# Performance work log

Measured on AMD Instinct MI355X. Metric: run time of the kernel, lower is better.

Reference implementation:

```python
import jax, jax.numpy as jnp
import numpy as np

L = 32            # num_layers
R = 16            # lora_rank
P = L * 7         # 224 projections
D = 256           # encoder d_model
H = 4             # encoder heads
HD = D // H
FF = 2048         # TransformerEncoderLayer default dim_feedforward
PED = 512         # proj_embed_dim
HID = 4096
KV = 8 * (4096 // 32)   # 1024
INTER = 11008
VOCAB = 50000
NEG = -1e9

# projection index groups within the P=7*L ordering [q,k,v,o,gate,up,down]
IDX_A_HID = jnp.asarray((np.arange(L)[:, None] * 7 + np.array([0, 1, 2, 3, 4, 5])).reshape(-1))  # in_dim=4096
IDX_A_INT = jnp.asarray(np.arange(L) * 7 + 6)                                                    # in_dim=11008
IDX_B_HID = jnp.asarray((np.arange(L)[:, None] * 7 + np.array([0, 3, 6])).reshape(-1))           # out_dim=4096
IDX_B_KV  = jnp.asarray((np.arange(L)[:, None] * 7 + np.array([1, 2])).reshape(-1))              # out_dim=1024
IDX_B_INT = jnp.asarray((np.arange(L)[:, None] * 7 + np.array([4, 5])).reshape(-1))              # out_dim=11008


def _ln(x, g, b, eps=1e-5):
    m = jnp.mean(x, -1, keepdims=True)
    v = jnp.mean((x - m) ** 2, -1, keepdims=True)
    return (x - m) * jax.lax.rsqrt(v + eps) * g + b


def _enc_layer(x, pad, qw, qb, ow, ob, g1, b1, f1w, f1b, f2w, f2b, g2, b2):
    # post-norm TransformerEncoderLayer (torch default), relu FFN, eval mode (no dropout)
    Bsz, S, _ = x.shape
    qkv = x @ qw.T + qb                                  # [B,S,3D]
    q, k, v = jnp.split(qkv, 3, axis=-1)
    hd = lambda t: t.reshape(Bsz, S, H, HD).transpose(0, 2, 1, 3)
    q, k, v = hd(q), hd(k), hd(v)
    s = jnp.einsum('bhqd,bhkd->bhqk', q, k) / jnp.asarray(np.sqrt(HD), x.dtype)
    s = jnp.where(pad[:, None, None, :], NEG, s)
    a = jax.nn.softmax(s, -1)
    o = jnp.einsum('bhqk,bhkd->bhqd', a, v).transpose(0, 2, 1, 3).reshape(Bsz, S, D)
    x = _ln(x + o @ ow.T + ob, g1, b1)
    f = jax.nn.relu(x @ f1w.T + f1b) @ f2w.T + f2b
    return _ln(x + f, g2, b2)


def _forward(condition_ids, attention_mask, embed_table, enc_qkv_w, enc_qkv_b, enc_out_w, enc_out_b,
             enc_ln1_g, enc_ln1_b, enc_ff1_w, enc_ff1_b, enc_ff2_w, enc_ff2_b, enc_ln2_g, enc_ln2_b,
             proj_w, proj_b, a1_w, a1_b, a2_w, a2_b, b1_w, b1_b, b2_w, b2_b, scales):
    Bsz = condition_ids.shape[0]
    x = embed_table[condition_ids]                       # [B,S,256]
    pad = attention_mask == 0                            # key padding mask (~attention_mask)
    for l in range(3):
        x = _enc_layer(x, pad, enc_qkv_w[l], enc_qkv_b[l], enc_out_w[l], enc_out_b[l],
                       enc_ln1_g[l], enc_ln1_b[l], enc_ff1_w[l], enc_ff1_b[l],
                       enc_ff2_w[l], enc_ff2_b[l], enc_ln2_g[l], enc_ln2_b[l])
    am = attention_mask.astype(x.dtype)
    pooled = (x * am[..., None]).sum(1) / jnp.clip(am.sum(1, keepdims=True), 1.0)   # masked mean pool
    pe = (pooled @ proj_w.T + proj_b).reshape(Bsz, P, PED)                          # [B,224,512]

    def dec(w1, b1_, w2, b2_):
        return jax.nn.gelu(pe @ w1.T + b1_, approximate=False) @ w2.T + b2_

    A_base = dec(a1_w, a1_b, a2_w, a2_b).reshape(Bsz, P, R, 64)   # [B,P,r,64]
    B_base = dec(b1_w, b1_b, b2_w, b2_b).reshape(Bsz, P, 64, R)   # [B,P,64,r]
    sa, sb = scales[:, 0], scales[:, 1]

    def tile_A(idx, in_d):
        # all in_dims divisible by 64 => repeat(in_d//64+1)[:, :in_d] == exact tiling
        a = A_base[:, idx] * sa[idx][None, :, None, None]
        return jnp.tile(a, (1, 1, 1, in_d // 64))

    def tile_B(idx, out_d):
        b = B_base[:, idx] * sb[idx][None, :, None, None]
        return jnp.tile(b, (1, 1, out_d // 64, 1))

    return (tile_A(IDX_A_HID, HID), tile_A(IDX_A_INT, INTER),
            tile_B(IDX_B_HID, HID), tile_B(IDX_B_KV, KV), tile_B(IDX_B_INT, INTER))


def setup_inputs() -> dict:
    key = jax.random.key(0)
    ks = iter(jax.random.split(key, 40))
    rn = lambda shape, s=0.02: jax.random.normal(next(ks), shape, jnp.float32) * s
    Bsz, S = 4, 128
    return {
        'condition_ids': jax.random.randint(next(ks), (Bsz, S), 0, VOCAB),
        'attention_mask': jnp.ones((Bsz, S), jnp.int32),
        'embed_table': rn((VOCAB, D)),
        'enc_qkv_w': rn((3, 3 * D, D)), 'enc_qkv_b': rn((3, 3 * D)),
        'enc_out_w': rn((3, D, D)), 'enc_out_b': rn((3, D)),
        'enc_ln1_g': jnp.ones((3, D)), 'enc_ln1_b': jnp.zeros((3, D)),
        'enc_ff1_w': rn((3, FF, D)), 'enc_ff1_b': rn((3, FF)),
        'enc_ff2_w': rn((3, D, FF)), 'enc_ff2_b': rn((3, D)),
        'enc_ln2_g': jnp.ones((3, D)), 'enc_ln2_b': jnp.zeros((3, D)),
        'proj_w': rn((P * PED, D)), 'proj_b': rn((P * PED,)),
        'a1_w': rn((D, PED)), 'a1_b': rn((D,)),
        'a2_w': rn((R * 64, D)), 'a2_b': rn((R * 64,)),
        'b1_w': rn((D, PED)), 'b1_b': rn((D,)),
        'b2_w': rn((R * 64, D)), 'b2_b': rn((R * 64,)),
        'scales': jnp.full((P, 2), 0.01, jnp.float32),
    }


def reference(condition_ids, attention_mask, embed_table, enc_qkv_w, enc_qkv_b, enc_out_w, enc_out_b,
              enc_ln1_g, enc_ln1_b, enc_ff1_w, enc_ff1_b, enc_ff2_w, enc_ff2_b, enc_ln2_g, enc_ln2_b,
              proj_w, proj_b, a1_w, a1_b, a2_w, a2_b, b1_w, b1_b, b2_w, b2_b, scales):
    return _forward(condition_ids, attention_mask, embed_table, enc_qkv_w, enc_qkv_b, enc_out_w, enc_out_b,
                    enc_ln1_g, enc_ln1_b, enc_ff1_w, enc_ff1_b, enc_ff2_w, enc_ff2_b, enc_ln2_g, enc_ln2_b,
                    proj_w, proj_b, a1_w, a1_b, a2_w, a2_b, b1_w, b1_b, b2_w, b2_b, scales)
```

## Files before the change

kernel.cpp:

```cpp
#include <hip/hip_runtime.h>
#include <hip/hip_bf16.h>

typedef unsigned short u16;
typedef unsigned int u32;
typedef __attribute__((ext_vector_type(8))) short short8;
typedef __attribute__((ext_vector_type(4))) float floatx4;

__device__ __forceinline__ u16 f2bf(float f) {
  u32 x = __float_as_uint(f);
  x += 0x7FFFu + ((x >> 16) & 1u);
  return (u16)(x >> 16);
}
__device__ __forceinline__ u32 pk2(float lo, float hi) {
  return (u32)f2bf(lo) | ((u32)f2bf(hi) << 16);
}

__global__ void embed_kernel(const int* __restrict__ ids, const float* __restrict__ emb,
                             float* __restrict__ x) {
  int tok = blockIdx.x, d = threadIdx.x;
  x[tok * 256 + d] = emb[(size_t)ids[tok] * 256 + d];
}

template <int ACT, int SPLIT>
__global__ __launch_bounds__(256) void mfma_gemm_kernel(const float* __restrict__ A,
    const float* __restrict__ W, const float* __restrict__ bias, float* __restrict__ C,
    int M, int N, int K, int KS, int pstride) {
  __shared__ u16 Abf[64 * 32];
  __shared__ u16 Wbf[64 * 32];
  const int t = threadIdx.x;
  const int m0 = blockIdx.x * 64, n0 = blockIdx.y * 64;
  const int kz = blockIdx.z;
  const int srow = t >> 2, skc = (t & 3) * 8;
  const int w = t >> 6, lane = t & 63;
  const int q = lane >> 4, rr = lane & 15;
  floatx4 acc[4];
#pragma unroll
  for (int i = 0; i < 4; ++i) acc[i] = (floatx4){0.f, 0.f, 0.f, 0.f};

  const int kbeg = kz * KS, kend = kbeg + KS;
  for (int k0 = kbeg; k0 < kend; k0 += 32) {
    const float* ga = A + (size_t)(m0 + srow) * K + k0 + skc;
    const float* gw = W + (size_t)(n0 + srow) * K + k0 + skc;
    float4 a0 = *(const float4*)ga;
    float4 a1 = *(const float4*)(ga + 4);
    float4 w0 = *(const float4*)gw;
    float4 w1 = *(const float4*)(gw + 4);
    uint4 pa, pw;
    pa.x = pk2(a0.x, a0.y); pa.y = pk2(a0.z, a0.w);
    pa.z = pk2(a1.x, a1.y); pa.w = pk2(a1.z, a1.w);
    pw.x = pk2(w0.x, w0.y); pw.y = pk2(w0.z, w0.w);
    pw.z = pk2(w1.x, w1.y); pw.w = pk2(w1.z, w1.w);
    __syncthreads();
    *(uint4*)&Abf[srow * 32 + skc] = pa;
    *(uint4*)&Wbf[srow * 32 + skc] = pw;
    __syncthreads();
    short8 af = *(short8*)&Abf[(w * 16 + rr) * 32 + q * 8];
#pragma unroll
    for (int ct = 0; ct < 4; ++ct) {
      short8 bf = *(short8*)&Wbf[(ct * 16 + rr) * 32 + q * 8];
      acc[ct] = __builtin_amdgcn_mfma_f32_16x16x32_bf16(af, bf, acc[ct], 0, 0, 0);
    }
  }

  float* dst = SPLIT ? (C + (size_t)kz * pstride) : C;
#pragma unroll
  for (int ct = 0; ct < 4; ++ct) {
    int col = n0 + ct * 16 + rr;
#pragma unroll
    for (int r = 0; r < 4; ++r) {
      int row = m0 + w * 16 + q * 4 + r;
      float v = acc[ct][r];
      if (!SPLIT) {
        v += bias[col];
        if (ACT == 1) v = fmaxf(v, 0.f);
        if (ACT == 2) v = 0.5f * v * (1.f + erff(v * 0.70710678118654752f));
      }
      dst[(size_t)row * N + col] = v;
    }
  }
}

template <int ACT>
__global__ void red_bias_act_kernel(const float* __restrict__ parts, int nparts, int pstride,
                                    const float* __restrict__ bias, float* __restrict__ dst, int N) {
  int idx = blockIdx.x * 256 + threadIdx.x;
  float v = bias[idx % N];
  for (int p = 0; p < nparts; ++p) v += parts[(size_t)p * pstride + idx];
  if (ACT == 1) v = fmaxf(v, 0.f);
  if (ACT == 2) v = 0.5f * v * (1.f + erff(v * 0.70710678118654752f));
  dst[idx] = v;
}

__global__ __launch_bounds__(256) void attn_kernel(const float* __restrict__ qkv,
    const int* __restrict__ mask, float* __restrict__ o) {
  __shared__ float Klds[8192];
  __shared__ float Vlds[8192];
  const int blk = blockIdx.x;
  const int b = blk >> 7, h = (blk >> 5) & 3, qg = blk & 31;
  const int t = threadIdx.x;
  for (int i = t; i < 8192; i += 256) {
    int s = i >> 6, d = i & 63;
    size_t base = (size_t)(b * 128 + s) * 768 + h * 64 + d;
    Klds[(s << 6) + (d ^ (s & 31))] = qkv[base + 256];
    Vlds[i] = qkv[base + 512];
  }
  __syncthreads();
  const int wave = t >> 6, lane = t & 63;
  const int q = qg * 4 + wave;
  float qv = qkv[(size_t)(b * 128 + q) * 768 + h * 64 + lane];
  const int m0i = mask[b * 128 + lane];
  const int m1i = mask[b * 128 + 64 + lane];
  float s0 = 0.f, s1 = 0.f;
  const int sw = lane & 31;
  for (int d = 0; d < 64; ++d) {
    float qd = __shfl(qv, d);
    s0 += qd * Klds[(lane << 6) + (d ^ sw)];
    s1 += qd * Klds[((lane + 64) << 6) + (d ^ sw)];
  }
  s0 *= 0.125f; s1 *= 0.125f;
  if (m0i == 0) s0 = -1000000000.0f;
  if (m1i == 0) s1 = -1000000000.0f;
  float m = fmaxf(s0, s1);
  for (int off = 32; off; off >>= 1) m = fmaxf(m, __shfl_xor(m, off));
  float p0 = expf(s0 - m), p1 = expf(s1 - m);
  float sum = p0 + p1;
  for (int off = 32; off; off >>= 1) sum += __shfl_xor(sum, off);
  float rs = 1.f / sum;
  float acc = 0.f;
  for (int k = 0; k < 64; ++k) acc += __shfl(p0, k) * Vlds[(k << 6) + lane];
  for (int k = 0; k < 64; ++k) acc += __shfl(p1, k) * Vlds[((k + 64) << 6) + lane];
  o[(size_t)(b * 128 + q) * 256 + h * 64 + lane] = acc * rs;
}

__global__ __launch_bounds__(256) void add_ln_red_kernel(float* __restrict__ x,
    const float* __restrict__ parts, int nparts, int pstride, const float* __restrict__ bias,
    const float* __restrict__ g, const float* __restrict__ b) {
  int tok = blockIdx.x, t = threadIdx.x;
  int idx = tok * 256 + t;
  float r = x[idx] + bias[t];
  for (int p = 0; p < nparts; ++p) r += parts[(size_t)p * pstride + idx];
  float s = r, sq = r * r;
  for (int off = 32; off; off >>= 1) { s += __shfl_xor(s, off); sq += __shfl_xor(sq, off); }
  __shared__ float red[8];
  int wave = t >> 6, lane = t & 63;
  if (lane == 0) { red[wave] = s; red[4 + wave] = sq; }
  __syncthreads();
  float S = red[0] + red[1] + red[2] + red[3];
  float SQ = red[4] + red[5] + red[6] + red[7];
  float mean = S * (1.f / 256.f);
  float var = SQ * (1.f / 256.f) - mean * mean;
  float inv = 1.f / sqrtf(fmaxf(var, 0.f) + 1e-5f);
  x[idx] = (r - mean) * inv * g[t] + b[t];
}

__global__ void pool_kernel(const float* __restrict__ x, const int* __restrict__ mask,
                            float* __restrict__ pooled) {
  int b = blockIdx.x, d = threadIdx.x;
  float s = 0.f, c = 0.f;
  for (int ss = 0; ss < 128; ++ss) {
    float m = (float)mask[b * 128 + ss];
    s += m * x[(size_t)(b * 128 + ss) * 256 + d];
    c += m;
  }
  pooled[b * 256 + d] = s / fmaxf(c, 1.f);
}

__global__ __launch_bounds__(256) void proj_kernel(const float* __restrict__ pooled,
    const float* __restrict__ W, const float* __restrict__ bias, float* __restrict__ pe) {
  __shared__ float pl[1024];
  int t = threadIdx.x;
  for (int i = t; i < 1024; i += 256) pl[i] = pooled[i];
  __syncthreads();
  int wave = t >> 6, lane = t & 63;
  int half = lane >> 5, sl = lane & 31;
  int row = blockIdx.x * 8 + wave * 2 + half;
  float4 w0 = *(const float4*)(W + (size_t)row * 256 + sl * 8);
  float4 w1 = *(const float4*)(W + (size_t)row * 256 + sl * 8 + 4);
  float a0, a1, a2, a3;
#pragma unroll
  for (int bb = 0; bb < 4; ++bb) {
    const float* pp = &pl[bb * 256 + sl * 8];
    float v = w0.x * pp[0] + w0.y * pp[1] + w0.z * pp[2] + w0.w * pp[3]
            + w1.x * pp[4] + w1.y * pp[5] + w1.z * pp[6] + w1.w * pp[7];
    if (bb == 0) a0 = v; else if (bb == 1) a1 = v; else if (bb == 2) a2 = v; else a3 = v;
  }
#pragma unroll
  for (int off = 1; off < 32; off <<= 1) {
    a0 += __shfl_xor(a0, off); a1 += __shfl_xor(a1, off);
    a2 += __shfl_xor(a2, off); a3 += __shfl_xor(a3, off);
  }
  if (sl == 0) {
    float bv = bias[row];
    pe[0 * 114688 + row] = a0 + bv;
    pe[1 * 114688 + row] = a1 + bv;
    pe[2 * 114688 + row] = a2 + bv;
    pe[3 * 114688 + row] = a3 + bv;
  }
}

__global__ __launch_bounds__(256) void tile_a_kernel(const float* __restrict__ Abase,
    const float* __restrict__ scales, float* __restrict__ out, int nI, int ind,
    int pdiv, int pmul, int padd) {
  int row = blockIdx.x;
  int r = row & 15, bi = row >> 4;
  int i = bi % nI, b = bi / nI;
  int p = (i / pdiv) * 7 + (i % pdiv) * pmul + padd;
  float s = scales[2 * p];
  __shared__ float chunk[64];
  int t = threadIdx.x;
  if (t < 64) chunk[t] = Abase[((size_t)(b * 224 + p) * 16 + r) * 64 + t] * s;
  __syncthreads();
  size_t ob = (size_t)row * ind;
  for (int u = t; u * 4 < ind; u += 256) {
    int c0 = u * 4;
    float4 ov = *(const float4*)&chunk[c0 & 63];
    *(float4*)(out + ob + c0) = ov;
  }
}

__global__ __launch_bounds__(256) void tile_b_kernel(const float* __restrict__ Bbase,
    const float* __restrict__ scales, float* __restrict__ out, int nI, int ind, int nchunks,
    int pdiv, int pmul, int padd) {
  int blk = blockIdx.x;
  int cc = blk % nchunks, bi = blk / nchunks;
  int i = bi % nI, b = bi / nI;
  int p = (i / pdiv) * 7 + (i % pdiv) * pmul + padd;
  float s = scales[2 * p + 1];
  __shared__ float chunk[1024];
  int t = threadIdx.x;
  for (int e = t; e < 1024; e += 256) chunk[e] = Bbase[(size_t)(b * 224 + p) * 1024 + e] * s;
  __syncthreads();
  int cchunk16 = (ind / nchunks) * 16;
  size_t ob = (size_t)bi * ind * 16 + (size_t)cc * cchunk16;
  for (int u = t; u * 4 < cchunk16; u += 256) {
    int e0 = u * 4;
    int cabs = (cc * cchunk16 + e0) >> 4;
    int src = ((cabs & 63) << 4) + (e0 & 15);
    float4 ov = *(const float4*)&chunk[src];
    *(float4*)(out + ob + e0) = ov;
  }
}

extern "C" void kernel_launch(void* const* d_in, const int* in_sizes, int n_in,
                              void* d_out, int out_size, void* d_ws, size_t ws_size,
                              hipStream_t stream) {
  const int* ids     = (const int*)d_in[0];
  const int* mask    = (const int*)d_in[1];
  const float* emb   = (const float*)d_in[2];
  const float* qkv_w = (const float*)d_in[3];
  const float* qkv_b = (const float*)d_in[4];
  const float* out_w = (const float*)d_in[5];
  const float* out_b = (const float*)d_in[6];
  const float* ln1_g = (const float*)d_in[7];
  const float* ln1_b = (const float*)d_in[8];
  const float* ff1_w = (const float*)d_in[9];
  const float* ff1_b = (const float*)d_in[10];
  const float* ff2_w = (const float*)d_in[11];
  const float* ff2_b = (const float*)d_in[12];
  const float* ln2_g = (const float*)d_in[13];
  const float* ln2_b = (const float*)d_in[14];
  const float* proj_w = (const float*)d_in[15];
  const float* proj_b = (const float*)d_in[16];
  const float* a1_w = (const float*)d_in[17];
  const float* a1_b = (const float*)d_in[18];
  const float* a2_w = (const float*)d_in[19];
  const float* a2_b = (const float*)d_in[20];
  const float* b1_w = (const float*)d_in[21];
  const float* b1_b = (const float*)d_in[22];
  const float* b2_w = (const float*)d_in[23];
  const float* b2_b = (const float*)d_in[24];
  const float* scales = (const float*)d_in[25];

  float* w = (float*)d_ws;
  float* x      = w + 0;
  float* qkv    = w + 262144;
  float* attn_o = w + 655360;
  float* ff     = w + 786432;
  float* pooled = w + 1835008;
  float* pe     = w + 1836032;
  float* hA     = w + 2294784;
  float* hB     = w + 2524160;
  float* Abase  = w + 2753536;
  float* Bbase  = w + 3671040;
  float* parts  = w + 4588544;

  float* out = (float*)d_out;

  embed_kernel<<<512, 256, 0, stream>>>(ids, emb, x);
  for (int l = 0; l < 3; ++l) {
    mfma_gemm_kernel<0, 0><<<dim3(8, 12), 256, 0, stream>>>(
        x, qkv_w + l * 768 * 256, qkv_b + l * 768, qkv, 512, 768, 256, 256, 0);
    attn_kernel<<<512, 256, 0, stream>>>(qkv, mask, attn_o);
    mfma_gemm_kernel<0, 1><<<dim3(8, 4, 4), 256, 0, stream>>>(
        attn_o, out_w + l * 256 * 256, nullptr, parts, 512, 256, 256, 64, 131072);
    add_ln_red_kernel<<<512, 256, 0, stream>>>(x, parts, 4, 131072, out_b + l * 256,
                                               ln1_g + l * 256, ln1_b + l * 256);
    mfma_gemm_kernel<1, 0><<<dim3(8, 32), 256, 0, stream>>>(
        x, ff1_w + l * 2048 * 256, ff1_b + l * 2048, ff, 512, 2048, 256, 256, 0);
    mfma_gemm_kernel<0, 1><<<dim3(8, 4, 8), 256, 0, stream>>>(
        ff, ff2_w + l * 256 * 2048, nullptr, parts, 512, 256, 2048, 256, 131072);
    add_ln_red_kernel<<<512, 256, 0, stream>>>(x, parts, 8, 131072, ff2_b + l * 256,
                                               ln2_g + l * 256, ln2_b + l * 256);
  }
  pool_kernel<<<4, 256, 0, stream>>>(x, mask, pooled);
  proj_kernel<<<14336, 256, 0, stream>>>(pooled, proj_w, proj_b, pe);

  mfma_gemm_kernel<0, 1><<<dim3(14, 4, 4), 256, 0, stream>>>(
      pe, a1_w, nullptr, parts, 896, 256, 512, 128, 229376);
  red_bias_act_kernel<2><<<896, 256, 0, stream>>>(parts, 4, 229376, a1_b, hA, 256);
  mfma_gemm_kernel<0, 0><<<dim3(14, 16), 256, 0, stream>>>(
      hA, a2_w, a2_b, Abase, 896, 1024, 256, 256, 0);

  mfma_gemm_kernel<0, 1><<<dim3(14, 4, 4), 256, 0, stream>>>(
      pe, b1_w, nullptr, parts, 896, 256, 512, 128, 229376);
  red_bias_act_kernel<2><<<896, 256, 0, stream>>>(parts, 4, 229376, b1_b, hB, 256);
  mfma_gemm_kernel<0, 0><<<dim3(14, 16), 256, 0, stream>>>(
      hB, b2_w, b2_b, Bbase, 896, 1024, 256, 256, 0);

  tile_a_kernel<<<12288, 256, 0, stream>>>(Abase, scales, out, 192, 4096, 6, 1, 0);
  tile_a_kernel<<<2048, 256, 0, stream>>>(Abase, scales, out + 50331648ull, 32, 11008, 1, 0, 6);
  tile_b_kernel<<<3072, 256, 0, stream>>>(Bbase, scales, out + 72876032ull, 96, 4096, 8, 3, 3, 0);
  tile_b_kernel<<<512, 256, 0, stream>>>(Bbase, scales, out + 98041856ull, 64, 1024, 2, 2, 1, 1);
  tile_b_kernel<<<2048, 256, 0, stream>>>(Bbase, scales, out + 102236160ull, 64, 11008, 8, 2, 1, 4);
}
```

Measured before the change: 976.3 us.

## Double-buffer GEMM LDS staging, merge LoRA A/B branch GEMMs, read V directly

The GEMM kernel now prefetches the next K-slice into registers and ping-pongs two LDS buffers, dropping one barrier per iteration. The A and B hypernetwork branches are merged into single launches, selected by column split, with a dual reduce+GELU kernel writing a concatenated hidden buffer. The attention kernel no longer stages V in LDS and instead reads it from global memory per lane. This cuts launches and sync overhead, but uncoalesced-ish strided V loads could cost more than the saved LDS traffic.

```diff
diff --git a/kernel.cpp b/kernel.cpp
--- a/kernel.cpp
+++ b/kernel.cpp
@@ -22,14 +22,23 @@
 }
 
 template <int ACT, int SPLIT>
-__global__ __launch_bounds__(256) void mfma_gemm_kernel(const float* __restrict__ A,
-    const float* __restrict__ W, const float* __restrict__ bias, float* __restrict__ C,
-    int M, int N, int K, int KS, int pstride) {
-  __shared__ u16 Abf[64 * 32];
-  __shared__ u16 Wbf[64 * 32];
+__global__ __launch_bounds__(256) void mfma_gemm_kernel(
+    const float* __restrict__ A, int lda,
+    const float* __restrict__ Wa, const float* __restrict__ Wb, int nsplit, int koffb,
+    const float* __restrict__ biasa, const float* __restrict__ biasb,
+    float* __restrict__ Ca, float* __restrict__ Cb,
+    int N, int K, int KS, int pstride) {
+  __shared__ u16 Abf[2][64 * 32];
+  __shared__ u16 Wbf[2][64 * 32];
   const int t = threadIdx.x;
-  const int m0 = blockIdx.x * 64, n0 = blockIdx.y * 64;
+  const int m0 = blockIdx.x * 64;
+  int n0 = blockIdx.y * 64;
   const int kz = blockIdx.z;
+  const float* W = Wa;
+  const float* bias = biasa;
+  const float* Ain = A;
+  float* C = Ca;
+  if (n0 >= nsplit) { n0 -= nsplit; W = Wb; bias = biasb; C = Cb; Ain = A + koffb; }
   const int srow = t >> 2, skc = (t & 3) * 8;
   const int w = t >> 6, lane = t & 63;
   const int q = lane >> 4, rr = lane & 15;
@@ -38,28 +47,36 @@
   for (int i = 0; i < 4; ++i) acc[i] = (floatx4){0.f, 0.f, 0.f, 0.f};
 
   const int kbeg = kz * KS, kend = kbeg + KS;
+  const float* ga = Ain + (size_t)(m0 + srow) * lda + kbeg + skc;
+  const float* gw = W + (size_t)(n0 + srow) * K + kbeg + skc;
+  float4 a0 = *(const float4*)ga;
+  float4 a1 = *(const float4*)(ga + 4);
+  float4 w0 = *(const float4*)gw;
+  float4 w1 = *(const float4*)(gw + 4);
+  int buf = 0;
   for (int k0 = kbeg; k0 < kend; k0 += 32) {
-    const float* ga = A + (size_t)(m0 + srow) * K + k0 + skc;
-    const float* gw = W + (size_t)(n0 + srow) * K + k0 + skc;
-    float4 a0 = *(const float4*)ga;
-    float4 a1 = *(const float4*)(ga + 4);
-    float4 w0 = *(const float4*)gw;
-    float4 w1 = *(const float4*)(gw + 4);
     uint4 pa, pw;
     pa.x = pk2(a0.x, a0.y); pa.y = pk2(a0.z, a0.w);
     pa.z = pk2(a1.x, a1.y); pa.w = pk2(a1.z, a1.w);
     pw.x = pk2(w0.x, w0.y); pw.y = pk2(w0.z, w0.w);
     pw.z = pk2(w1.x, w1.y); pw.w = pk2(w1.z, w1.w);
+    *(uint4*)&Abf[buf][t * 8] = pa;
+    *(uint4*)&Wbf[buf][t * 8] = pw;
+    if (k0 + 32 < kend) {
+      ga += 32; gw += 32;
+      a0 = *(const float4*)ga;
+      a1 = *(const float4*)(ga + 4);
+      w0 = *(const float4*)gw;
+      w1 = *(const float4*)(gw + 4);
+    }
     __syncthreads();
-    *(uint4*)&Abf[srow * 32 + skc] = pa;
-    *(uint4*)&Wbf[srow * 32 + skc] = pw;
-    __syncthreads();
-    short8 af = *(short8*)&Abf[(w * 16 + rr) * 32 + q * 8];
+    short8 af = *(short8*)&Abf[buf][(w * 16 + rr) * 32 + q * 8];
 #pragma unroll
     for (int ct = 0; ct < 4; ++ct) {
-      short8 bf = *(short8*)&Wbf[(ct * 16 + rr) * 32 + q * 8];
-      acc[ct] = __builtin_amdgcn_mfma_f32_16x16x32_bf16(af, bf, acc[ct], 0, 0, 0);
+      short8 bfv = *(short8*)&Wbf[buf][(ct * 16 + rr) * 32 + q * 8];
+      acc[ct] = __builtin_amdgcn_mfma_f32_16x16x32_bf16(af, bfv, acc[ct], 0, 0, 0);
     }
+    buf ^= 1;
   }
 
   float* dst = SPLIT ? (C + (size_t)kz * pstride) : C;
@@ -80,29 +97,31 @@
   }
 }
 
-template <int ACT>
-__global__ void red_bias_act_kernel(const float* __restrict__ parts, int nparts, int pstride,
-                                    const float* __restrict__ bias, float* __restrict__ dst, int N) {
-  int idx = blockIdx.x * 256 + threadIdx.x;
-  float v = bias[idx % N];
-  for (int p = 0; p < nparts; ++p) v += parts[(size_t)p * pstride + idx];
-  if (ACT == 1) v = fmaxf(v, 0.f);
-  if (ACT == 2) v = 0.5f * v * (1.f + erff(v * 0.70710678118654752f));
-  dst[idx] = v;
+__global__ __launch_bounds__(256) void red_gelu_dual_kernel(const float* __restrict__ pa,
+    const float* __restrict__ pb, const float* __restrict__ ba, const float* __restrict__ bb,
+    float* __restrict__ h) {
+  int blk = blockIdx.x;
+  int second = blk >= 896;
+  int row = second ? blk - 896 : blk;
+  const float* parts = second ? pb : pa;
+  const float* bias = second ? bb : ba;
+  int c = threadIdx.x;
+  float v = bias[c];
+#pragma unroll
+  for (int p = 0; p < 4; ++p) v += parts[(size_t)p * 229376 + row * 256 + c];
+  v = 0.5f * v * (1.f + erff(v * 0.70710678118654752f));
+  h[(size_t)row * 512 + second * 256 + c] = v;
 }
 
 __global__ __launch_bounds__(256) void attn_kernel(const float* __restrict__ qkv,
     const int* __restrict__ mask, float* __restrict__ o) {
   __shared__ float Klds[8192];
-  __shared__ float Vlds[8192];
   const int blk = blockIdx.x;
   const int b = blk >> 7, h = (blk >> 5) & 3, qg = blk & 31;
   const int t = threadIdx.x;
   for (int i = t; i < 8192; i += 256) {
     int s = i >> 6, d = i & 63;
-    size_t base = (size_t)(b * 128 + s) * 768 + h * 64 + d;
-    Klds[(s << 6) + (d ^ (s & 31))] = qkv[base + 256];
-    Vlds[i] = qkv[base + 512];
+    Klds[(s << 6) + (d ^ (s & 31))] = qkv[(size_t)(b * 128 + s) * 768 + h * 64 + 256 + d];
   }
   __syncthreads();
   const int wave = t >> 6, lane = t & 63;
@@ -126,9 +145,12 @@
   float sum = p0 + p1;
   for (int off = 32; off; off >>= 1) sum += __shfl_xor(sum, off);
   float rs = 1.f / sum;
+  const float* vb = qkv + (size_t)b * 98304 + h * 64 + 512 + lane;
   float acc = 0.f;
-  for (int k = 0; k < 64; ++k) acc += __shfl(p0, k) * Vlds[(k << 6) + lane];
-  for (int k = 0; k < 64; ++k) acc += __shfl(p1, k) * Vlds[((k + 64) << 6) + lane];
+#pragma unroll
+  for (int k = 0; k < 64; ++k) acc += __shfl(p0, k) * vb[(size_t)k * 768];
+#pragma unroll
+  for (int k = 0; k < 64; ++k) acc += __shfl(p1, k) * vb[(size_t)(k + 64) * 768];
   o[(size_t)(b * 128 + q) * 256 + h * 64 + lane] = acc * rs;
 }
 
@@ -278,44 +300,44 @@
   float* ff     = w + 786432;
   float* pooled = w + 1835008;
   float* pe     = w + 1836032;
-  float* hA     = w + 2294784;
-  float* hB     = w + 2524160;
+  float* hbuf   = w + 2294784;
   float* Abase  = w + 2753536;
   float* Bbase  = w + 3671040;
   float* parts  = w + 4588544;
 
   float* out = (float*)d_out;
+  const int NSB = 1 << 30;
 
   embed_kernel<<<512, 256, 0, stream>>>(ids, emb, x);
   for (int l = 0; l < 3; ++l) {
     mfma_gemm_kernel<0, 0><<<dim3(8, 12), 256, 0, stream>>>(
-        x, qkv_w + l * 768 * 256, qkv_b + l * 768, qkv, 512, 768, 256, 256, 0);
+        x, 256, qkv_w + l * 768 * 256, nullptr, NSB, 0, qkv_b + l * 768, nullptr,
+        qkv, nullptr, 768, 256, 256, 0);
     attn_kernel<<<512, 256, 0, stream>>>(qkv, mask, attn_o);
     mfma_gemm_kernel<0, 1><<<dim3(8, 4, 4), 256, 0, stream>>>(
-        attn_o, out_w + l * 256 * 256, nullptr, parts, 512, 256, 256, 64, 131072);
+        attn_o, 256, out_w + l * 256 * 256, nullptr, NSB, 0, nullptr, nullptr,
+        parts, nullptr, 256, 256, 64, 131072);
     add_ln_red_kernel<<<512, 256, 0, stream>>>(x, parts, 4, 131072, out_b + l * 256,
                                                ln1_g + l * 256, ln1_b + l * 256);
     mfma_gemm_kernel<1, 0><<<dim3(8, 32), 256, 0, stream>>>(
-        x, ff1_w + l * 2048 * 256, ff1_b + l * 2048, ff, 512, 2048, 256, 256, 0);
+        x, 256, ff1_w + l * 2048 * 256, nullptr, NSB, 0, ff1_b + l * 2048, nullptr,
+        ff, nullptr, 2048, 256, 256, 0);
     mfma_gemm_kernel<0, 1><<<dim3(8, 4, 8), 256, 0, stream>>>(
-        ff, ff2_w + l * 256 * 2048, nullptr, parts, 512, 256, 2048, 256, 131072);
+        ff, 2048, ff2_w + l * 256 * 2048, nullptr, NSB, 0, nullptr, nullptr,
+        parts, nullptr, 256, 2048, 256, 131072);
     add_ln_red_kernel<<<512, 256, 0, stream>>>(x, parts, 8, 131072, ff2_b + l * 256,
                                                ln2_g + l * 256, ln2_b + l * 256);
   }
   pool_kernel<<<4, 256, 0, stream>>>(x, mask, pooled);
   proj_kernel<<<14336, 256, 0, stream>>>(pooled, proj_w, proj_b, pe);
 
-  mfma_gemm_kernel<0, 1><<<dim3(14, 4, 4), 256, 0, stream>>>(
-      pe, a1_w, nullptr, parts, 896, 256, 512, 128, 229376);
-  red_bias_act_kernel<2><<<896, 256, 0, stream>>>(parts, 4, 229376, a1_b, hA, 256);
-  mfma_gemm_kernel<0, 0><<<dim3(14, 16), 256, 0, stream>>>(
-      hA, a2_w, a2_b, Abase, 896, 1024, 256, 256, 0);
-
-  mfma_gemm_kernel<0, 1><<<dim3(14, 4, 4), 256, 0, stream>>>(
-      pe, b1_w, nullptr, parts, 896, 256, 512, 128, 229376);
-  red_bias_act_kernel<2><<<896, 256, 0, stream>>>(parts, 4, 229376, b1_b, hB, 256);
-  mfma_gemm_kernel<0, 0><<<dim3(14, 16), 256, 0, stream>>>(
-      hB, b2_w, b2_b, Bbase, 896, 1024, 256, 256, 0);
+  mfma_gemm_kernel<0, 1><<<dim3(14, 8, 4), 256, 0, stream>>>(
+      pe, 512, a1_w, b1_w, 256, 0, nullptr, nullptr,
+      parts, ff, 256, 512, 128, 229376);
+  red_gelu_dual_kernel<<<1792, 256, 0, stream>>>(parts, ff, a1_b, b1_b, hbuf);
+  mfma_gemm_kernel<0, 0><<<dim3(14, 32), 256, 0, stream>>>(
+      hbuf, 512, a2_w, b2_w, 1024, 256, a2_b, b2_b,
+      Abase, Bbase, 1024, 256, 256, 0);
 
   tile_a_kernel<<<12288, 256, 0, stream>>>(Abase, scales, out, 192, 4096, 6, 1, 0);
   tile_a_kernel<<<2048, 256, 0, stream>>>(Abase, scales, out + 50331648ull, 32, 11008, 1, 0, 6);
```

After: 921.7 us. 1.06x faster.
